# Optimization experiments

Measured on AMD Instinct MI355X. Metric: run time of the kernel, lower is better.

The kernel has to match this reference:

```python
import jax, jax.numpy as jnp
import numpy as np

N = 10000      # nodes
E = 160000     # edges (avg degree 16)
H = 128        # hidden_size
L = 3          # n_layers
NRBF = 20
RADIUS = 5.0
EPS = 1e-8
MAXZ = 100


def _xav(k, shape):
    fan_in = shape[-2]
    return jax.random.normal(k, shape, jnp.float32) / jnp.sqrt(jnp.float32(fan_in))


def setup_inputs() -> dict:
    key = jax.random.key(0)
    ks = jax.random.split(key, 12)
    return {
        "z": jax.random.randint(ks[0], (N,), 0, MAXZ, dtype=jnp.int32),
        "edge_vec": jax.random.normal(ks[1], (E, 3), jnp.float32),
        "senders": jax.random.randint(ks[2], (E,), 0, N, dtype=jnp.int32),
        "receivers": jax.random.randint(ks[3], (E,), 0, N, dtype=jnp.int32),
        "emb": jax.random.uniform(ks[4], (MAXZ, H), jnp.float32, -0.1, 0.1),
        "filt_W": _xav(ks[5], (NRBF, L * 3 * H)),
        "filt_b": jnp.zeros((L * 3 * H,), jnp.float32),
        "iW1": _xav(ks[6], (L, H, H)),
        "ib1": jnp.zeros((L, H), jnp.float32),
        "iW2": _xav(ks[7], (L, H, 3 * H)),
        "ib2": jnp.zeros((L, 3 * H), jnp.float32),
        "mW1": _xav(ks[8], (L, 2 * H, H)),
        "mb1": jnp.zeros((L, H), jnp.float32),
        "mW2": _xav(ks[9], (L, H, 3 * H)),
        "mb2": jnp.zeros((L, 3 * H), jnp.float32),
        "vW": _xav(ks[10], (L, H, 2 * H)),
    }


def _painn(z, edge_vec, senders, receivers, emb, filt_W, filt_b,
           iW1, ib1, iW2, ib2, mW1, mb1, mW2, mb2, vW):
    n = z.shape[0]
    clip = lambda x: jnp.clip(x, -1e4, 1e4)

    # edge geometry: norm + direction
    d = jnp.sqrt(jnp.sum(edge_vec ** 2, axis=-1, keepdims=True) + EPS)  # [E,1]
    dir_ij = edge_vec / d                                               # [E,3]

    # gaussian radial basis + cosine cutoff
    mu = jnp.linspace(0.0, RADIUS, NRBF)
    gamma = 0.5 / (RADIUS / NRBF) ** 2
    phi = jnp.exp(-gamma * (d - mu) ** 2)                               # [E,NRBF]
    cut = 0.5 * (jnp.cos(jnp.pi * d / RADIUS) + 1.0) * (d < RADIUS)     # [E,1]

    filters = (phi @ filt_W + filt_b) * cut                             # [E, L*3H]
    filt = jnp.split(filters, L, axis=-1)

    # embed
    s = emb[z]                                                          # [N,H]
    v = jnp.zeros((n, 3, H), dtype=s.dtype)                             # [N,3,H]

    for l in range(L):
        # ---- message ----
        x = jax.nn.silu(s @ iW1[l] + ib1[l]) @ iW2[l] + ib2[l]          # [N,3H]
        m = filt[l] * x[receivers]                                      # [E,3H]
        ds, dv1, dv2 = jnp.split(m, 3, axis=-1)
        dv = dv1[:, None, :] * dir_ij[:, :, None] + dv2[:, None, :] * v[receivers]  # [E,3,H]
        ds = jax.ops.segment_sum(ds, senders, num_segments=n)
        dv = jax.ops.segment_sum(dv, senders, num_segments=n)
        s = s + clip(ds)
        v = v + clip(dv)
        # ---- update / mixing ----
        v_l, v_r = jnp.split(v @ vW[l], 2, axis=-1)                     # [N,3,H] each
        v_norm = jnp.sqrt(jnp.sum(v_l ** 2, axis=-2) + EPS)             # [N,H]
        ts = jnp.concatenate([s, v_norm], axis=-1)                      # [N,2H]
        mm = jax.nn.silu(ts @ mW1[l] + mb1[l]) @ mW2[l] + mb2[l]        # [N,3H]
        ds2, dvu, dsv = jnp.split(mm, 3, axis=-1)
        s = s + clip(ds2 + dsv * jnp.sum(v_l * v_r, axis=1))
        v = v + clip(dvu[:, None, :] * v_r)
    return s, v


def reference(z, edge_vec, senders, receivers, emb, filt_W, filt_b,
              iW1, ib1, iW2, ib2, mW1, mb1, mW2, mb2, vW):
    return _painn(z, edge_vec, senders, receivers, emb, filt_W, filt_b,
                  iW1, ib1, iW2, ib2, mW1, mb1, mW2, mb2, vW)
```

## Files before the change

### kernel.cpp

```cpp
#include <hip/hip_runtime.h>
#include <math.h>

#define NN 10000
#define EE 160000
#define H 128
#define LAYERS 3
#define NRBF 20
#define RADIUS 5.0f
#define PI_F 3.14159265358979323846f

using f16    = _Float16;
using h2     = __attribute__((ext_vector_type(2)))  _Float16;
using half8  = __attribute__((ext_vector_type(8)))  _Float16;
using f32x16 = __attribute__((ext_vector_type(16))) float;
using u32x4  = __attribute__((ext_vector_type(4)))  unsigned int;

__device__ __forceinline__ float clipf(float x){ return fminf(fmaxf(x, -1e4f), 1e4f); }
__device__ __forceinline__ float siluf(float x){ return x / (1.0f + __expf(-x)); }

__global__ __launch_bounds__(256) void hist_kernel(const int* __restrict__ send, int* __restrict__ cnt){
    int e = blockIdx.x * 256 + threadIdx.x;
    if (e < EE) atomicAdd(&cnt[send[e]], 1);
}

__global__ __launch_bounds__(1024) void scan_kernel(const int* __restrict__ cnt,
                                                    int* __restrict__ row_ptr,
                                                    int* __restrict__ cursor){
    __shared__ int part[1024];
    int t = threadIdx.x;
    int base = t * 10;
    int local[10];
    int sum = 0;
    #pragma unroll
    for (int i = 0; i < 10; i++){
        int idx = base + i;
        local[i] = (idx < NN) ? cnt[idx] : 0;
        sum += local[i];
    }
    part[t] = sum;
    __syncthreads();
    for (int off = 1; off < 1024; off <<= 1){
        int val = (t >= off) ? part[t - off] : 0;
        __syncthreads();
        part[t] += val;
        __syncthreads();
    }
    int run = (t > 0) ? part[t-1] : 0;
    #pragma unroll
    for (int i = 0; i < 10; i++){
        int idx = base + i;
        if (idx < NN){ row_ptr[idx] = run; cursor[idx] = run; run += local[i]; }
    }
    if (t == 1023) row_ptr[NN] = part[1023];
}

__global__ __launch_bounds__(256) void build_kernel(const float* __restrict__ ev,
                                                    const int* __restrict__ send,
                                                    const int* __restrict__ recv,
                                                    int* __restrict__ cursor,
                                                    int* __restrict__ recv_s,
                                                    f16* __restrict__ Ps){
    int e = blockIdx.x * 256 + threadIdx.x;
    if (e >= EE) return;
    int p = atomicAdd(&cursor[send[e]], 1);
    recv_s[p] = recv[e];
    float x = ev[e*3+0], y = ev[e*3+1], z = ev[e*3+2];
    float d = sqrtf(x*x + y*y + z*z + 1e-8f);
    float inv = 1.0f / d;
    float cut = (d < RADIUS) ? 0.5f * (__cosf(PI_F * d / RADIUS) + 1.0f) : 0.0f;
    union { u32x4 q[3]; f16 h[24]; } o;
    #pragma unroll
    for (int k = 0; k < NRBF; k++){
        float mu = RADIUS * (float)k / (float)(NRBF - 1);
        float t = d - mu;
        o.h[k] = (f16)(__expf(-8.0f * t * t) * cut);
    }
    o.h[20] = (f16)cut;
    o.h[21] = (f16)(x*inv); o.h[22] = (f16)(y*inv); o.h[23] = (f16)(z*inv);
    u32x4* dst = (u32x4*)(Ps + (size_t)p*24);
    dst[0] = o.q[0]; dst[1] = o.q[1]; dst[2] = o.q[2];
}

__global__ __launch_bounds__(256) void wconv_kernel(const float* __restrict__ iW1, const float* __restrict__ iW2,
                                                    const float* __restrict__ vW,  const float* __restrict__ mW1,
                                                    const float* __restrict__ mW2,
                                                    f16* __restrict__ iW1T, f16* __restrict__ iW2T,
                                                    f16* __restrict__ vWT,  f16* __restrict__ mW1T,
                                                    f16* __restrict__ mW2T){
    int idx = blockIdx.x*256 + threadIdx.x;
    if (idx >= 3*180224) return;
    int l = idx / 180224;
    int r = idx % 180224;
    float val; f16* dst;
    if (r < 16384){
        int n = r >> 7, k = r & 127;
        val = iW1[l*16384 + k*128 + n]; dst = iW1T + l*16384 + r;
    } else if (r < 65536){
        int r2 = r - 16384; int n = r2 >> 7, k = r2 & 127;
        val = iW2[l*49152 + k*384 + n]; dst = iW2T + l*49152 + r2;
    } else if (r < 98304){
        int r2 = r - 65536; int n = r2 >> 7, k = r2 & 127;
        val = vW[l*32768 + k*256 + n]; dst = vWT + l*32768 + r2;
    } else if (r < 131072){
        int r2 = r - 98304; int n = r2 >> 8, k = r2 & 255;
        val = mW1[l*32768 + k*128 + n]; dst = mW1T + l*32768 + r2;
    } else {
        int r2 = r - 131072; int n = r2 >> 7, k = r2 & 127;
        val = mW2[l*49152 + k*384 + n]; dst = mW2T + l*49152 + r2;
    }
    *dst = (f16)val;
}

__global__ __launch_bounds__(256) void embed_kernel(const int* __restrict__ z,
                                                    const float* __restrict__ emb,
                                                    float* __restrict__ s, f16* __restrict__ sh){
    int idx = blockIdx.x * 256 + threadIdx.x;
    if (idx >= NN * H) return;
    int n = idx >> 7, h = idx & 127;
    float val = emb[z[n]*H + h];
    s[idx] = val;
    sh[idx] = (f16)val;
}

__global__ __launch_bounds__(256) void mlp1_kernel(const f16* __restrict__ A,
                                                   const f16* __restrict__ W1T,
                                                   const float* __restrict__ b1,
                                                   const f16* __restrict__ W2T,
                                                   const float* __restrict__ b2,
                                                   f16* __restrict__ out){
    __shared__ f16 As[32][136];
    __shared__ f16 Hs[32][136];
    int t = threadIdx.x;
    int n0 = blockIdx.x * 32;
    for (int i = t; i < 512; i += 256){
        int row = i >> 4, k8 = (i & 15) * 8;
        half8 val = {};
        if (n0 + row < NN) val = *(const half8*)(A + (size_t)(n0+row)*128 + k8);
        *(half8*)&As[row][k8] = val;
    }
    __syncthreads();
    int lane = t & 63, w = t >> 6;
    int ar = lane & 31;
    int koff = (lane >> 5) * 8;
    {
        int bcol = w*32 + ar;
        const f16* bp = W1T + (size_t)bcol*128 + koff;
        f32x16 acc = {};
        #pragma unroll
        for (int kc = 0; kc < 8; kc++){
            half8 bf = *(const half8*)(bp + kc*16);
            half8 a  = *(const half8*)(&As[ar][koff + kc*16]);
            acc = __builtin_amdgcn_mfma_f32_32x32x16_f16(a, bf, acc, 0, 0, 0);
        }
        float bv = b1[bcol];
        #pragma unroll
        for (int r = 0; r < 16; r++){
            int row = (r&3) + 8*(r>>2) + 4*(lane>>5);
            Hs[row][bcol] = (f16)siluf(acc[r] + bv);
        }
    }
    __syncthreads();
    #pragma unroll
    for (int cc = 0; cc < 3; cc++){
        int bcol = (w + cc*4)*32 + ar;
        const f16* bp = W2T + (size_t)bcol*128 + koff;
        f32x16 acc = {};
        #pragma unroll
        for (int kc = 0; kc < 8; kc++){
            half8 bf = *(const half8*)(bp + kc*16);
            half8 a  = *(const half8*)(&Hs[ar][koff + kc*16]);
            acc = __builtin_amdgcn_mfma_f32_32x32x16_f16(a, bf, acc, 0, 0, 0);
        }
        float bv = b2[bcol];
        #pragma unroll
        for (int r = 0; r < 16; r++){
            int row = (r&3) + 8*(r>>2) + 4*(lane>>5);
            int g = n0 + row;
            if (g < NN) out[(size_t)g*384 + bcol] = (f16)(acc[r] + bv);
        }
    }
}

__global__ __launch_bounds__(128) void msg_kernel(const f16* __restrict__ Ps,
                                                  const int* __restrict__ recv_s,
                                                  const int* __restrict__ row_ptr,
                                                  const f16* __restrict__ xh,
                                                  const f16* __restrict__ vh,
                                                  const float* __restrict__ fW, const float* __restrict__ fb,
                                                  float* __restrict__ s, f16* __restrict__ sh,
                                                  float* __restrict__ v, f16* __restrict__ v2h, int l){
    int t = threadIdx.x;
    int lane = t & 63;
    int n = blockIdx.x * 2 + (t >> 6);
    int h0 = lane * 2;
    int col0 = l*384 + h0;
    h2 wf0[NRBF], wf1[NRBF], wf2[NRBF];
    #pragma unroll
    for (int k = 0; k < NRBF; k++){
        const float* w = fW + k*1152 + col0;
        wf0[k] = h2{(f16)w[0],   (f16)w[1]};
        wf1[k] = h2{(f16)w[128], (f16)w[129]};
        wf2[k] = h2{(f16)w[256], (f16)w[257]};
    }
    float b0x = fb[col0],     b0y = fb[col0+1];
    float b1x = fb[col0+128], b1y = fb[col0+129];
    float b2x = fb[col0+256], b2y = fb[col0+257];
    int beg = row_ptr[n], end = row_ptr[n+1];
    float ds0=0.f, ds1=0.f, dv00=0.f, dv01=0.f, dv10=0.f, dv11=0.f, dv20=0.f, dv21=0.f;
    #pragma unroll 2
    for (int idx = beg; idx < end; idx++){
        const u32x4* pp = (const u32x4*)(Ps + (size_t)idx*24);
        union { u32x4 q[3]; f16 ph[24]; } u;
        u.q[0] = pp[0]; u.q[1] = pp[1]; u.q[2] = pp[2];
        int r = recv_s[idx];
        h2 f0 = {}, f1 = {}, f2 = {};
        #pragma unroll
        for (int k = 0; k < NRBF; k++){
            f16 pk = u.ph[k];
            h2 pk2 = h2{pk, pk};
            f0 += pk2 * wf0[k];
            f1 += pk2 * wf1[k];
            f2 += pk2 * wf2[k];
        }
        float cut = (float)u.ph[20];
        float F00 = fmaf(b0x, cut, (float)f0.x), F01 = fmaf(b0y, cut, (float)f0.y);
        float F10 = fmaf(b1x, cut, (float)f1.x), F11 = fmaf(b1y, cut, (float)f1.y);
        float F20 = fmaf(b2x, cut, (float)f2.x), F21 = fmaf(b2y, cut, (float)f2.y);
        const f16* xr = xh + (size_t)r*384 + h0;
        h2 X0 = *(const h2*)xr;
        h2 X1 = *(const h2*)(xr + 128);
        h2 X2 = *(const h2*)(xr + 256);
        const f16* vp = vh + (size_t)r*128 + h0;
        h2 V0 = *(const h2*)vp;
        h2 V1 = *(const h2*)(vp + (size_t)NN*128);
        h2 V2 = *(const h2*)(vp + (size_t)2*NN*128);
        float d0 = (float)u.ph[21], d1 = (float)u.ph[22], d2 = (float)u.ph[23];
        ds0 = fmaf(F00, (float)X0.x, ds0);
        float a0 = F10 * (float)X1.x, bb0 = F20 * (float)X2.x;
        dv00 = fmaf(a0, d0, fmaf(bb0, (float)V0.x, dv00));
        dv10 = fmaf(a0, d1, fmaf(bb0, (float)V1.x, dv10));
        dv20 = fmaf(a0, d2, fmaf(bb0, (float)V2.x, dv20));
        ds1 = fmaf(F01, (float)X0.y, ds1);
        float a1 = F11 * (float)X1.y, bb1 = F21 * (float)X2.y;
        dv01 = fmaf(a1, d0, fmaf(bb1, (float)V0.y, dv01));
        dv11 = fmaf(a1, d1, fmaf(bb1, (float)V1.y, dv11));
        dv21 = fmaf(a1, d2, fmaf(bb1, (float)V2.y, dv21));
    }
    int si = n*H + h0;
    float sv0 = s[si]   + clipf(ds0);
    float sv1 = s[si+1] + clipf(ds1);
    s[si] = sv0; s[si+1] = sv1;
    *(h2*)&sh[si] = h2{(f16)sv0, (f16)sv1};
    size_t vb = (size_t)n*384 + h0;
    float nv00 = v[vb]     + clipf(dv00), nv01 = v[vb+1]   + clipf(dv01);
    float nv10 = v[vb+128] + clipf(dv10), nv11 = v[vb+129] + clipf(dv11);
    float nv20 = v[vb+256] + clipf(dv20), nv21 = v[vb+257] + clipf(dv21);
    v[vb] = nv00;     v[vb+1] = nv01;
    v[vb+128] = nv10; v[vb+129] = nv11;
    v[vb+256] = nv20; v[vb+257] = nv21;
    size_t pb = (size_t)n*128 + h0;
    *(h2*)&v2h[pb]                    = h2{(f16)nv00, (f16)nv01};
    *(h2*)&v2h[pb + (size_t)NN*128]   = h2{(f16)nv10, (f16)nv11};
    *(h2*)&v2h[pb + (size_t)2*NN*128] = h2{(f16)nv20, (f16)nv21};
}

__global__ __launch_bounds__(256) void vmix_kernel(const f16* __restrict__ v2h,
                                                   const f16* __restrict__ sh_in,
                                                   const f16* __restrict__ vWT,
                                                   const f16* __restrict__ W1T,
                                                   const float* __restrict__ b1,
                                                   const f16* __restrict__ W2T,
                                                   const float* __restrict__ b2,
                                                   float* __restrict__ s, f16* __restrict__ sh,
                                                   float* __restrict__ v, f16* __restrict__ vh){
    __shared__ f16 As3[3][32][136];
    __shared__ f16 ts[32][264];
    __shared__ f16 Hs[32][136];
    int t = threadIdx.x;
    int n0 = blockIdx.x * 32;
    for (int i = t; i < 1536; i += 256){
        int c = i / 512; int rem = i - c*512; int row = rem >> 4; int k8 = (rem & 15) * 8;
        half8 val = {};
        if (n0 + row < NN) val = *(const half8*)(v2h + ((size_t)c*NN + n0 + row)*128 + k8);
        *(half8*)&As3[c][row][k8] = val;
    }
    for (int i = t; i < 512; i += 256){
        int row = i >> 4, k8 = (i & 15) * 8;
        half8 val = {};
        if (n0 + row < NN) val = *(const half8*)(sh_in + (size_t)(n0+row)*128 + k8);
        *(half8*)&ts[row][k8] = val;
    }
    __syncthreads();
    int lane = t & 63, w = t >> 6;
    int ar = lane & 31;
    int koff = (lane >> 5) * 8;
    int jl = w*32 + ar;
    f32x16 al[3], arr[3];
    #pragma unroll
    for (int c = 0; c < 3; c++){
        f32x16 accl = {}, accr = {};
        #pragma unroll
        for (int kc = 0; kc < 8; kc++){
            half8 bl = *(const half8*)(vWT + (size_t)jl*128 + koff + kc*16);
            half8 br = *(const half8*)(vWT + (size_t)(128+jl)*128 + koff + kc*16);
            half8 a  = *(const half8*)(&As3[c][ar][koff + kc*16]);
            accl = __builtin_amdgcn_mfma_f32_32x32x16_f16(a, bl, accl, 0, 0, 0);
            accr = __builtin_amdgcn_mfma_f32_32x32x16_f16(a, br, accr, 0, 0, 0);
        }
        al[c] = accl; arr[c] = accr;
    }
    float dot[16], vr0[16], vr1[16], vr2[16];
    #pragma unroll
    for (int r = 0; r < 16; r++){
        int row = (r&3) + 8*(r>>2) + 4*(lane>>5);
        float l0=al[0][r], l1=al[1][r], l2=al[2][r];
        float r0=arr[0][r], r1=arr[1][r], r2=arr[2][r];
        ts[row][128 + jl] = (f16)sqrtf(l0*l0 + l1*l1 + l2*l2 + 1e-8f);
        dot[r] = l0*r0 + l1*r1 + l2*r2;
        vr0[r] = r0; vr1[r] = r1; vr2[r] = r2;
    }
    __syncthreads();
    {
        int bcol = w*32 + ar;
        const f16* bp = W1T + (size_t)bcol*256 + koff;
        f32x16 acc = {};
        #pragma unroll
        for (int kc = 0; kc < 16; kc++){
            half8 bf = *(const half8*)(bp + kc*16);
            half8 a  = *(const half8*)(&ts[ar][koff + kc*16]);
            acc = __builtin_amdgcn_mfma_f32_32x32x16_f16(a, bf, acc, 0, 0, 0);
        }
        float bv = b1[bcol];
        #pragma unroll
        for (int r = 0; r < 16; r++){
            int row = (r&3) + 8*(r>>2) + 4*(lane>>5);
            Hs[row][bcol] = (f16)siluf(acc[r] + bv);
        }
    }
    __syncthreads();
    f32x16 macc[3];
    #pragma unroll
    for (int cc = 0; cc < 3; cc++){
        int bcol = (w + cc*4)*32 + ar;
        const f16* bp = W2T + (size_t)bcol*128 + koff;
        f32x16 acc = {};
        #pragma unroll
        for (int kc = 0; kc < 8; kc++){
            half8 bf = *(const half8*)(bp + kc*16);
            half8 a  = *(const half8*)(&Hs[ar][koff + kc*16]);
            acc = __builtin_amdgcn_mfma_f32_32x32x16_f16(a, bf, acc, 0, 0, 0);
        }
        macc[cc] = acc;
    }
    int jj = w*32 + ar;
    float bv0 = b2[jj], bv1 = b2[128 + jj], bv2 = b2[256 + jj];
    #pragma unroll
    for (int r = 0; r < 16; r++){
        int node = n0 + (r&3) + 8*(r>>2) + 4*(lane>>5);
        if (node < NN){
            float m0 = macc[0][r] + bv0;
            float m1 = macc[1][r] + bv1;
            float m2 = macc[2][r] + bv2;
            size_t si = (size_t)node*128 + jj;
            float sv = s[si] + clipf(m0 + m2*dot[r]);
            s[si] = sv; sh[si] = (f16)sv;
            size_t vi = (size_t)node*384 + jj;
            float nv0 = v[vi]       + clipf(m1 * vr0[r]);
            float nv1 = v[vi + 128] + clipf(m1 * vr1[r]);
            float nv2 = v[vi + 256] + clipf(m1 * vr2[r]);
            v[vi]       = nv0;
            v[vi + 128] = nv1;
            v[vi + 256] = nv2;
            vh[si]                    = (f16)nv0;
            vh[si + (size_t)NN*128]   = (f16)nv1;
            vh[si + (size_t)2*NN*128] = (f16)nv2;
        }
    }
}

extern "C" void kernel_launch(void* const* d_in, const int* in_sizes, int n_in,
                              void* d_out, int out_size, void* d_ws, size_t ws_size,
                              hipStream_t stream) {
    const int*   z    = (const int*)  d_in[0];
    const float* ev   = (const float*)d_in[1];
    const int*   send = (const int*)  d_in[2];
    const int*   recv = (const int*)  d_in[3];
    const float* emb  = (const float*)d_in[4];
    const float* fW   = (const float*)d_in[5];
    const float* fb   = (const float*)d_in[6];
    const float* iW1  = (const float*)d_in[7];
    const float* ib1  = (const float*)d_in[8];
    const float* iW2  = (const float*)d_in[9];
    const float* ib2  = (const float*)d_in[10];
    const float* mW1  = (const float*)d_in[11];
    const float* mb1  = (const float*)d_in[12];
    const float* mW2  = (const float*)d_in[13];
    const float* mb2  = (const float*)d_in[14];
    const float* vW   = (const float*)d_in[15];

    float* s = (float*)d_out;
    float* v = s + NN*H;

    char* base = (char*)d_ws;
    f16*   Ps     = (f16*)base;   base += (size_t)EE*24*2;
    int*   recvs  = (int*)base;   base += (size_t)EE*4;
    f16*   xh     = (f16*)base;   base += (size_t)NN*384*2;
    f16*   v2h    = (f16*)base;   base += (size_t)3*NN*128*2;
    f16*   vh     = (f16*)base;   base += (size_t)3*NN*128*2;
    f16*   sh     = (f16*)base;   base += (size_t)NN*128*2;
    f16*   iW1T   = (f16*)base;   base += (size_t)3*16384*2;
    f16*   iW2T   = (f16*)base;   base += (size_t)3*49152*2;
    f16*   vWT    = (f16*)base;   base += (size_t)3*32768*2;
    f16*   mW1T   = (f16*)base;   base += (size_t)3*32768*2;
    f16*   mW2T   = (f16*)base;   base += (size_t)3*49152*2;
    int* cnt      = (int*)base;   base += (size_t)NN*4;
    int* row_ptr  = (int*)base;   base += (size_t)(NN+1)*4;
    int* cursor   = (int*)base;

    hipMemsetAsync(cnt, 0, NN*sizeof(int), stream);
    hist_kernel<<<(EE+255)/256, 256, 0, stream>>>(send, cnt);
    scan_kernel<<<1, 1024, 0, stream>>>(cnt, row_ptr, cursor);
    build_kernel<<<(EE+255)/256, 256, 0, stream>>>(ev, send, recv, cursor, recvs, Ps);
    wconv_kernel<<<(3*180224+255)/256, 256, 0, stream>>>(iW1, iW2, vW, mW1, mW2,
                                                         iW1T, iW2T, vWT, mW1T, mW2T);
    embed_kernel<<<(NN*H+255)/256, 256, 0, stream>>>(z, emb, s, sh);
    hipMemsetAsync(v,  0, (size_t)NN*384*sizeof(float), stream);
    hipMemsetAsync(vh, 0, (size_t)3*NN*128*sizeof(f16), stream);

    const int MB32 = (NN + 31) / 32;

    for (int l = 0; l < LAYERS; l++){
        mlp1_kernel<<<MB32, 256, 0, stream>>>(sh, iW1T + l*16384, ib1 + l*H,
                                              iW2T + l*49152, ib2 + l*384, xh);
        msg_kernel<<<NN/2, 128, 0, stream>>>(Ps, recvs, row_ptr, xh, vh, fW, fb, s, sh, v, v2h, l);
        vmix_kernel<<<MB32, 256, 0, stream>>>(v2h, sh, vWT + l*32768,
                                              mW1T + l*32768, mb1 + l*H,
                                              mW2T + l*49152, mb2 + l*384,
                                              s, sh, v, vh);
    }
}
```

Before: 373.8 us.

## Fuse next-layer interaction MLP into vmix and software-prefetch edge gathers in msg

The next layer's interaction MLP (two MFMA GEMMs producing xh) now runs at the end of vmix_kernel, reusing the freshly updated s tile held in shared memory. This removes a separate mlp1 launch per layer and the reload of sh. Separately, the msg_kernel edge loop now double-buffers its loads: the next edge's packed RBF data, receiver features and v are fetched while the current edge is computed, to hide gather latency. The cost is higher register pressure and extra shared-memory syncs in vmix.

```diff
diff --git a/kernel.cpp b/kernel.cpp
--- a/kernel.cpp
+++ b/kernel.cpp
@@ -207,44 +207,59 @@
     float b2x = fb[col0+256], b2y = fb[col0+257];
     int beg = row_ptr[n], end = row_ptr[n+1];
     float ds0=0.f, ds1=0.f, dv00=0.f, dv01=0.f, dv10=0.f, dv11=0.f, dv20=0.f, dv21=0.f;
-    #pragma unroll 2
-    for (int idx = beg; idx < end; idx++){
-        const u32x4* pp = (const u32x4*)(Ps + (size_t)idx*24);
-        union { u32x4 q[3]; f16 ph[24]; } u;
-        u.q[0] = pp[0]; u.q[1] = pp[1]; u.q[2] = pp[2];
-        int r = recv_s[idx];
-        h2 f0 = {}, f1 = {}, f2 = {};
-        #pragma unroll
-        for (int k = 0; k < NRBF; k++){
-            f16 pk = u.ph[k];
-            h2 pk2 = h2{pk, pk};
-            f0 += pk2 * wf0[k];
-            f1 += pk2 * wf1[k];
-            f2 += pk2 * wf2[k];
-        }
-        float cut = (float)u.ph[20];
-        float F00 = fmaf(b0x, cut, (float)f0.x), F01 = fmaf(b0y, cut, (float)f0.y);
-        float F10 = fmaf(b1x, cut, (float)f1.x), F11 = fmaf(b1y, cut, (float)f1.y);
-        float F20 = fmaf(b2x, cut, (float)f2.x), F21 = fmaf(b2y, cut, (float)f2.y);
-        const f16* xr = xh + (size_t)r*384 + h0;
-        h2 X0 = *(const h2*)xr;
-        h2 X1 = *(const h2*)(xr + 128);
-        h2 X2 = *(const h2*)(xr + 256);
-        const f16* vp = vh + (size_t)r*128 + h0;
-        h2 V0 = *(const h2*)vp;
-        h2 V1 = *(const h2*)(vp + (size_t)NN*128);
-        h2 V2 = *(const h2*)(vp + (size_t)2*NN*128);
-        float d0 = (float)u.ph[21], d1 = (float)u.ph[22], d2 = (float)u.ph[23];
-        ds0 = fmaf(F00, (float)X0.x, ds0);
-        float a0 = F10 * (float)X1.x, bb0 = F20 * (float)X2.x;
-        dv00 = fmaf(a0, d0, fmaf(bb0, (float)V0.x, dv00));
-        dv10 = fmaf(a0, d1, fmaf(bb0, (float)V1.x, dv10));
-        dv20 = fmaf(a0, d2, fmaf(bb0, (float)V2.x, dv20));
-        ds1 = fmaf(F01, (float)X0.y, ds1);
-        float a1 = F11 * (float)X1.y, bb1 = F21 * (float)X2.y;
-        dv01 = fmaf(a1, d0, fmaf(bb1, (float)V0.y, dv01));
-        dv11 = fmaf(a1, d1, fmaf(bb1, (float)V1.y, dv11));
-        dv21 = fmaf(a1, d2, fmaf(bb1, (float)V2.y, dv21));
+    if (beg < end){
+        int r2 = (beg+1 < end) ? recv_s[beg+1] : 0;
+        const u32x4* pp0 = (const u32x4*)(Ps + (size_t)beg*24);
+        u32x4 q0n = pp0[0], q1n = pp0[1], q2n = pp0[2];
+        int r1 = recv_s[beg];
+        const f16* xp0 = xh + (size_t)r1*384 + h0;
+        h2 X0n = *(const h2*)xp0, X1n = *(const h2*)(xp0+128), X2n = *(const h2*)(xp0+256);
+        const f16* vp0 = vh + (size_t)r1*128 + h0;
+        h2 V0n = *(const h2*)vp0;
+        h2 V1n = *(const h2*)(vp0 + (size_t)NN*128);
+        h2 V2n = *(const h2*)(vp0 + (size_t)2*NN*128);
+        for (int idx = beg; idx < end; idx++){
+            union { u32x4 q[3]; f16 ph[24]; } u;
+            u.q[0] = q0n; u.q[1] = q1n; u.q[2] = q2n;
+            h2 X0 = X0n, X1 = X1n, X2 = X2n, V0 = V0n, V1 = V1n, V2 = V2n;
+            int i1 = idx + 1;
+            if (i1 < end){
+                const u32x4* pn = (const u32x4*)(Ps + (size_t)i1*24);
+                q0n = pn[0]; q1n = pn[1]; q2n = pn[2];
+                int rg = r2;
+                const f16* xn = xh + (size_t)rg*384 + h0;
+                X0n = *(const h2*)xn; X1n = *(const h2*)(xn+128); X2n = *(const h2*)(xn+256);
+                const f16* vn = vh + (size_t)rg*128 + h0;
+                V0n = *(const h2*)vn;
+                V1n = *(const h2*)(vn + (size_t)NN*128);
+                V2n = *(const h2*)(vn + (size_t)2*NN*128);
+                r2 = (idx+2 < end) ? recv_s[idx+2] : rg;
+            }
+            h2 f0 = {}, f1 = {}, f2 = {};
+            #pragma unroll
+            for (int k = 0; k < NRBF; k++){
+                f16 pk = u.ph[k];
+                h2 pk2 = h2{pk, pk};
+                f0 += pk2 * wf0[k];
+                f1 += pk2 * wf1[k];
+                f2 += pk2 * wf2[k];
+            }
+            float cut = (float)u.ph[20];
+            float F00 = fmaf(b0x, cut, (float)f0.x), F01 = fmaf(b0y, cut, (float)f0.y);
+            float F10 = fmaf(b1x, cut, (float)f1.x), F11 = fmaf(b1y, cut, (float)f1.y);
+            float F20 = fmaf(b2x, cut, (float)f2.x), F21 = fmaf(b2y, cut, (float)f2.y);
+            float d0 = (float)u.ph[21], d1 = (float)u.ph[22], d2 = (float)u.ph[23];
+            ds0 = fmaf(F00, (float)X0.x, ds0);
+            float a0 = F10 * (float)X1.x, bb0 = F20 * (float)X2.x;
+            dv00 = fmaf(a0, d0, fmaf(bb0, (float)V0.x, dv00));
+            dv10 = fmaf(a0, d1, fmaf(bb0, (float)V1.x, dv10));
+            dv20 = fmaf(a0, d2, fmaf(bb0, (float)V2.x, dv20));
+            ds1 = fmaf(F01, (float)X0.y, ds1);
+            float a1 = F11 * (float)X1.y, bb1 = F21 * (float)X2.y;
+            dv01 = fmaf(a1, d0, fmaf(bb1, (float)V0.y, dv01));
+            dv11 = fmaf(a1, d1, fmaf(bb1, (float)V1.y, dv11));
+            dv21 = fmaf(a1, d2, fmaf(bb1, (float)V2.y, dv21));
+        }
     }
     int si = n*H + h0;
     float sv0 = s[si]   + clipf(ds0);
@@ -264,6 +279,7 @@
     *(h2*)&v2h[pb + (size_t)2*NN*128] = h2{(f16)nv20, (f16)nv21};
 }
 
+template<bool FUSE>
 __global__ __launch_bounds__(256) void vmix_kernel(const f16* __restrict__ v2h,
                                                    const f16* __restrict__ sh_in,
                                                    const f16* __restrict__ vWT,
@@ -271,8 +287,13 @@
                                                    const float* __restrict__ b1,
                                                    const f16* __restrict__ W2T,
                                                    const float* __restrict__ b2,
+                                                   const f16* __restrict__ iW1Tn,
+                                                   const float* __restrict__ ib1n,
+                                                   const f16* __restrict__ iW2Tn,
+                                                   const float* __restrict__ ib2n,
                                                    float* __restrict__ s, f16* __restrict__ sh,
-                                                   float* __restrict__ v, f16* __restrict__ vh){
+                                                   float* __restrict__ v, f16* __restrict__ vh,
+                                                   f16* __restrict__ xh){
     __shared__ f16 As3[3][32][136];
     __shared__ f16 ts[32][264];
     __shared__ f16 Hs[32][136];
@@ -356,7 +377,8 @@
     float bv0 = b2[jj], bv1 = b2[128 + jj], bv2 = b2[256 + jj];
     #pragma unroll
     for (int r = 0; r < 16; r++){
-        int node = n0 + (r&3) + 8*(r>>2) + 4*(lane>>5);
+        int row = (r&3) + 8*(r>>2) + 4*(lane>>5);
+        int node = n0 + row;
         if (node < NN){
             float m0 = macc[0][r] + bv0;
             float m1 = macc[1][r] + bv1;
@@ -364,6 +386,7 @@
             size_t si = (size_t)node*128 + jj;
             float sv = s[si] + clipf(m0 + m2*dot[r]);
             s[si] = sv; sh[si] = (f16)sv;
+            if (FUSE) ts[row][jj] = (f16)sv;
             size_t vi = (size_t)node*384 + jj;
             float nv0 = v[vi]       + clipf(m1 * vr0[r]);
             float nv1 = v[vi + 128] + clipf(m1 * vr1[r]);
@@ -374,6 +397,47 @@
             vh[si]                    = (f16)nv0;
             vh[si + (size_t)NN*128]   = (f16)nv1;
             vh[si + (size_t)2*NN*128] = (f16)nv2;
+        } else if (FUSE){
+            ts[row][jj] = (f16)0.0f;
+        }
+    }
+    if (!FUSE) return;
+    __syncthreads();
+    {
+        int bcol = w*32 + ar;
+        const f16* bp = iW1Tn + (size_t)bcol*128 + koff;
+        f32x16 acc = {};
+        #pragma unroll
+        for (int kc = 0; kc < 8; kc++){
+            half8 bf = *(const half8*)(bp + kc*16);
+            half8 a  = *(const half8*)(&ts[ar][koff + kc*16]);
+            acc = __builtin_amdgcn_mfma_f32_32x32x16_f16(a, bf, acc, 0, 0, 0);
+        }
+        float bv = ib1n[bcol];
+        #pragma unroll
+        for (int r = 0; r < 16; r++){
+            int row = (r&3) + 8*(r>>2) + 4*(lane>>5);
+            Hs[row][bcol] = (f16)siluf(acc[r] + bv);
+        }
+    }
+    __syncthreads();
+    #pragma unroll
+    for (int cc = 0; cc < 3; cc++){
+        int bcol = (w + cc*4)*32 + ar;
+        const f16* bp = iW2Tn + (size_t)bcol*128 + koff;
+        f32x16 acc = {};
+        #pragma unroll
+        for (int kc = 0; kc < 8; kc++){
+            half8 bf = *(const half8*)(bp + kc*16);
+            half8 a  = *(const half8*)(&Hs[ar][koff + kc*16]);
+            acc = __builtin_amdgcn_mfma_f32_32x32x16_f16(a, bf, acc, 0, 0, 0);
+        }
+        float bv = ib2n[bcol];
+        #pragma unroll
+        for (int r = 0; r < 16; r++){
+            int row = (r&3) + 8*(r>>2) + 4*(lane>>5);
+            int g = n0 + row;
+            if (g < NN) xh[(size_t)g*384 + bcol] = (f16)(acc[r] + bv);
         }
     }
 }
@@ -429,13 +493,22 @@
 
     const int MB32 = (NN + 31) / 32;
 
+    mlp1_kernel<<<MB32, 256, 0, stream>>>(sh, iW1T, ib1, iW2T, ib2, xh);
     for (int l = 0; l < LAYERS; l++){
-        mlp1_kernel<<<MB32, 256, 0, stream>>>(sh, iW1T + l*16384, ib1 + l*H,
-                                              iW2T + l*49152, ib2 + l*384, xh);
         msg_kernel<<<NN/2, 128, 0, stream>>>(Ps, recvs, row_ptr, xh, vh, fW, fb, s, sh, v, v2h, l);
-        vmix_kernel<<<MB32, 256, 0, stream>>>(v2h, sh, vWT + l*32768,
-                                              mW1T + l*32768, mb1 + l*H,
-                                              mW2T + l*49152, mb2 + l*384,
-                                              s, sh, v, vh);
-    }
-}
+        if (l < LAYERS-1){
+            vmix_kernel<true><<<MB32, 256, 0, stream>>>(v2h, sh, vWT + l*32768,
+                                                        mW1T + l*32768, mb1 + l*H,
+                                                        mW2T + l*49152, mb2 + l*384,
+                                                        iW1T + (l+1)*16384, ib1 + (l+1)*H,
+                                                        iW2T + (l+1)*49152, ib2 + (l+1)*384,
+                                                        s, sh, v, vh, xh);
+        } else {
+            vmix_kernel<false><<<MB32, 256, 0, stream>>>(v2h, sh, vWT + l*32768,
+                                                         mW1T + l*32768, mb1 + l*H,
+                                                         mW2T + l*49152, mb2 + l*384,
+                                                         nullptr, nullptr, nullptr, nullptr,
+                                                         s, sh, v, vh, xh);
+        }
+    }
+}
```

Result: slower. 399.9 us (+7.0%).
